# Performance work log

Measured on AMD Instinct MI355X. Metric: run time of the kernel, lower is better.

## Reference

```python
import jax, jax.numpy as jnp
import numpy as np

N = 50000      # nodes (cells)
E = 800000     # directed edges
IN, H1, H2, Z = 512, 128, 128, 64


def setup_inputs() -> dict:
    key = jax.random.key(0)
    ks = jax.random.split(key, 12)
    x = jax.random.normal(ks[0], (N, IN), jnp.float32)
    edge_index = jax.random.randint(ks[1], (2, E), 0, N, dtype=jnp.int64)

    def glorot(k, i, o):
        return jax.random.normal(k, (i, o), jnp.float32) * np.float32(1.0 / np.sqrt(i))

    return {
        "x": x,
        "edge_index": edge_index,
        "W1": glorot(ks[2], IN, H1), "b1": jnp.zeros((H1,), jnp.float32),
        "W2": glorot(ks[3], H1, H2), "b2": jnp.zeros((H2,), jnp.float32),
        "Wm": glorot(ks[4], H2, Z),  "bm": jnp.zeros((Z,), jnp.float32),
        "Ws": glorot(ks[5], H2, Z),  "bs": jnp.zeros((Z,), jnp.float32),
    }


def _gcn_norm(edge_index, n):
    # PyG GCNConv default: add self-loops, sym-normalize D^-1/2 (A+I) D^-1/2
    loops = jnp.arange(n, dtype=edge_index.dtype)
    src = jnp.concatenate([edge_index[0], loops])
    dst = jnp.concatenate([edge_index[1], loops])
    deg = jax.ops.segment_sum(jnp.ones_like(dst, jnp.float32), dst, num_segments=n)
    dis = jnp.where(deg > 0, jax.lax.rsqrt(jnp.maximum(deg, 1.0)), 0.0)
    norm = dis[src] * dis[dst]  # [E+N]
    return src, dst, norm


def _gcn_conv(x, W, b, src, dst, norm, n):
    h = x @ W                          # [N, out] transform first
    msg = h[src] * norm[:, None]       # gather + scale
    out = jax.ops.segment_sum(msg, dst, num_segments=n)  # scatter-add at targets
    return out + b


def reference(x, edge_index, W1, b1, W2, b2, Wm, bm, Ws, bs):
    n = x.shape[0]
    src, dst, norm = _gcn_norm(edge_index, n)
    h = jax.nn.relu(_gcn_conv(x, W1, b1, src, dst, norm, n))
    h = jax.nn.relu(_gcn_conv(h, W2, b2, src, dst, norm, n))
    # dropout p=0.4 is identity in eval mode
    z_mean = _gcn_conv(h, Wm, bm, src, dst, norm, n)
    z_log_std = _gcn_conv(h, Ws, bs, src, dst, norm, n)
    return (z_mean, z_log_std)
```

## Files before the change

kernel.cpp:

```cpp
#include <hip/hip_runtime.h>


using u16 = unsigned short;
typedef __attribute__((ext_vector_type(8))) short short8;
typedef __attribute__((ext_vector_type(4))) float f32x4;

__device__ __forceinline__ void split_bf16(float f, u16& hi, u16& lo) {
    unsigned b = __float_as_uint(f);
    hi = (u16)(b >> 16);
    float rem = f - __uint_as_float(b & 0xFFFF0000u);
    lo = (u16)(__float_as_uint(rem) >> 16);
}

__device__ __forceinline__ int block_mode(const int* __restrict__ ew, int* sflag) {
    if (threadIdx.x == 0) *sflag = 0;
    __syncthreads();
    if (ew[2 * (int)threadIdx.x + 1] != 0) atomicOr(sflag, 1);
    __syncthreads();
    return *sflag ? 0 : 1;
}

__global__ void deg_kernel(const int* __restrict__ ew, int* __restrict__ deg, int E) {
    __shared__ int sflag;
    int mode = block_mode(ew, &sflag);
    int e = blockIdx.x * blockDim.x + threadIdx.x;
    if (e >= E) return;
    int d = mode ? ew[2 * E + 2 * e] : ew[E + e];
    atomicAdd(&deg[d], 1);
}

__global__ void scan_block_kernel(const int* __restrict__ deg, int* __restrict__ rowptr,
                                  int* __restrict__ aux, float* __restrict__ dis, int N) {
    __shared__ int s[256];
    int i = blockIdx.x * 256 + threadIdx.x;
    int v = (i < N) ? deg[i] : 0;
    if (i < N) dis[i] = rsqrtf((float)v + 1.0f);
    s[threadIdx.x] = v;
    __syncthreads();
    for (int off = 1; off < 256; off <<= 1) {
        int t = (threadIdx.x >= off) ? s[threadIdx.x - off] : 0;
        __syncthreads();
        s[threadIdx.x] += t;
        __syncthreads();
    }
    if (i < N) rowptr[i] = s[threadIdx.x] - v;
    if (threadIdx.x == 255) aux[blockIdx.x] = s[255];
}

__global__ void scan_aux_kernel(int* __restrict__ aux, int nb) {
    __shared__ int s[256];
    int i = threadIdx.x;
    int v = (i < nb) ? aux[i] : 0;
    s[i] = v;
    __syncthreads();
    for (int off = 1; off < 256; off <<= 1) {
        int t = (i >= off) ? s[i - off] : 0;
        __syncthreads();
        s[i] += t;
        __syncthreads();
    }
    if (i < nb) aux[i] = s[i] - v;
}

__global__ void add_offsets_kernel(int* __restrict__ rowptr, const int* __restrict__ aux,
                                   int N, int E) {
    int i = blockIdx.x * 256 + threadIdx.x;
    if (i < N) rowptr[i] += aux[i >> 8];
    if (i == 0) rowptr[N] = E;
}

__global__ void fill_csr_kernel(const int* __restrict__ ew,
                                const int* __restrict__ rowptr, int* __restrict__ cursor,
                                int* __restrict__ csr_src, int E) {
    __shared__ int sflag;
    int mode = block_mode(ew, &sflag);
    int e = blockIdx.x * blockDim.x + threadIdx.x;
    if (e >= E) return;
    int s = mode ? ew[2 * e] : ew[e];
    int d = mode ? ew[2 * E + 2 * e] : ew[E + e];
    int pos = rowptr[d] + atomicAdd(&cursor[d], 1);
    csr_src[pos] = s;
}

__global__ void conv_all_kernel(const float* __restrict__ W1, const float* __restrict__ W2,
                                const float* __restrict__ Wm, const float* __restrict__ Ws,
                                u16* __restrict__ W1t_hi, u16* __restrict__ W1t_lo,
                                u16* __restrict__ W2t_hi, u16* __restrict__ W2t_lo,
                                u16* __restrict__ Wct_hi, u16* __restrict__ Wct_lo) {
    int idx = blockIdx.x * 256 + threadIdx.x;
    u16 h, l;
    if (idx < 65536) {
        int k = idx >> 7, n = idx & 127;
        split_bf16(W1[idx], h, l);
        W1t_hi[n * 512 + k] = h;
        W1t_lo[n * 512 + k] = l;
    } else if (idx < 81920) {
        int t = idx - 65536;
        int k = t >> 7, n = t & 127;
        split_bf16(W2[t], h, l);
        W2t_hi[n * 128 + k] = h;
        W2t_lo[n * 128 + k] = l;
    } else if (idx < 98304) {
        int t = idx - 81920;
        int k = t >> 7, j = t & 127;
        float f = (j < 64) ? Wm[k * 64 + j] : Ws[k * 64 + (j - 64)];
        split_bf16(f, h, l);
        Wct_hi[j * 128 + k] = h;
        Wct_lo[j * 128 + k] = l;
    }
}

#define TILE_OFF(t) ((t) * 520)

__global__ __launch_bounds__(256) void gemm_mfma(const float* __restrict__ A,
                                                 const u16* __restrict__ Bt_hi,
                                                 const u16* __restrict__ Bt_lo,
                                                 float* __restrict__ C,
                                                 int N, int K) {
    __shared__ u16 AsH[4 * 520], AsL[4 * 520];
    __shared__ u16 BsH[8 * 520], BsL[8 * 520];

    const int tid = threadIdx.x;
    const int w = tid >> 6, lane = tid & 63;
    const int row0 = blockIdx.y * 64;

    const int s_ar = w * 16 + (lane & 15);
    const int s_ak = (lane >> 4) * 8;
    const int a_dst = TILE_OFF(w) + lane * 8;
    const int s_bc = tid >> 1;
    const int s_bk = (tid & 1) * 16;
    const int b_q0 = (tid & 1) * 2;
    const int b_dst0 = TILE_OFF(s_bc >> 4) + ((s_bc & 15) + 16 * (b_q0 + 0)) * 8;
    const int b_dst1 = TILE_OFF(s_bc >> 4) + ((s_bc & 15) + 16 * (b_q0 + 1)) * 8;

    const int R = (w >> 1) * 32, Cc = (w & 1) * 64;
    const int atile = (w >> 1) * 2;
    const int btile = (w & 1) * 4;
    const int m16 = lane & 15, quad = lane >> 4;

    f32x4 acc[2][4];
#pragma unroll
    for (int i = 0; i < 2; ++i)
#pragma unroll
        for (int j = 0; j < 4; ++j) acc[i][j] = (f32x4)0.f;

    const int grow = row0 + s_ar;
    const bool ok = (grow < N);
    const float* aptr = A + (size_t)grow * K + s_ak;
    const u16* bph = Bt_hi + (size_t)s_bc * K + s_bk;
    const u16* bpl = Bt_lo + (size_t)s_bc * K + s_bk;

    float av[8];
    short8 rbh0, rbh1, rbl0, rbl1;
    {
        f32x4 v0 = (f32x4)0.f, v1 = (f32x4)0.f;
        if (ok) { v0 = *(const f32x4*)&aptr[0]; v1 = *(const f32x4*)&aptr[4]; }
#pragma unroll
        for (int q = 0; q < 4; ++q) { av[q] = v0[q]; av[4 + q] = v1[q]; }
        rbh0 = *(const short8*)&bph[0];
        rbh1 = *(const short8*)&bph[8];
        rbl0 = *(const short8*)&bpl[0];
        rbl1 = *(const short8*)&bpl[8];
    }

    const int ksteps = K >> 5;
    for (int ks = 0; ks < ksteps; ++ks) {
        short8 ah, al;
#pragma unroll
        for (int q = 0; q < 8; ++q) {
            u16 h, l;
            split_bf16(av[q], h, l);
            ah[q] = (short)h;
            al[q] = (short)l;
        }
        __syncthreads();
        *(short8*)&AsH[a_dst] = ah;
        *(short8*)&AsL[a_dst] = al;
        *(short8*)&BsH[b_dst0] = rbh0;
        *(short8*)&BsH[b_dst1] = rbh1;
        *(short8*)&BsL[b_dst0] = rbl0;
        *(short8*)&BsL[b_dst1] = rbl1;
        __syncthreads();

        if (ks + 1 < ksteps) {
            const int k0 = (ks + 1) * 32;
            f32x4 v0 = (f32x4)0.f, v1 = (f32x4)0.f;
            if (ok) { v0 = *(const f32x4*)&aptr[k0]; v1 = *(const f32x4*)&aptr[k0 + 4]; }
#pragma unroll
            for (int q = 0; q < 4; ++q) { av[q] = v0[q]; av[4 + q] = v1[q]; }
            rbh0 = *(const short8*)&bph[k0];
            rbh1 = *(const short8*)&bph[k0 + 8];
            rbl0 = *(const short8*)&bpl[k0];
            rbl1 = *(const short8*)&bpl[k0 + 8];
        }

        short8 fa_h[2], fa_l[2], fb_h[4], fb_l[4];
#pragma unroll
        for (int i = 0; i < 2; ++i) {
            fa_h[i] = *(const short8*)&AsH[TILE_OFF(atile + i) + lane * 8];
            fa_l[i] = *(const short8*)&AsL[TILE_OFF(atile + i) + lane * 8];
        }
#pragma unroll
        for (int j = 0; j < 4; ++j) {
            fb_h[j] = *(const short8*)&BsH[TILE_OFF(btile + j) + lane * 8];
            fb_l[j] = *(const short8*)&BsL[TILE_OFF(btile + j) + lane * 8];
        }
#pragma unroll
        for (int i = 0; i < 2; ++i)
#pragma unroll
            for (int j = 0; j < 4; ++j) {
                acc[i][j] = __builtin_amdgcn_mfma_f32_16x16x32_bf16(
                    fa_h[i], fb_h[j], acc[i][j], 0, 0, 0);
                acc[i][j] = __builtin_amdgcn_mfma_f32_16x16x32_bf16(
                    fa_h[i], fb_l[j], acc[i][j], 0, 0, 0);
                acc[i][j] = __builtin_amdgcn_mfma_f32_16x16x32_bf16(
                    fa_l[i], fb_h[j], acc[i][j], 0, 0, 0);
            }
    }

#pragma unroll
    for (int i = 0; i < 2; ++i) {
#pragma unroll
        for (int r = 0; r < 4; ++r) {
            int gr = row0 + R + i * 16 + quad * 4 + r;
            if (gr < N) {
#pragma unroll
                for (int j = 0; j < 4; ++j)
                    C[(size_t)gr * 128 + Cc + j * 16 + m16] = acc[i][j][r];
            }
        }
    }
}

__global__ __launch_bounds__(256) void propagate_kernel(
    const float* __restrict__ h, const int* __restrict__ rowptr,
    const int* __restrict__ csr_src, const float* __restrict__ dis,
    const float* __restrict__ bias, float* __restrict__ out, int N, int do_relu) {
    int wave = (blockIdx.x * 256 + threadIdx.x) >> 6;
    int lane = threadIdx.x & 63;
    if (wave >= N) return;
    int v = wave;
    int f = lane * 2;
    float dv = dis[v];
    float ax = 0.f, ay = 0.f;
    int beg = rowptr[v], end = rowptr[v + 1];
    int i = beg;
    for (; i + 8 <= end; i += 8) {
        int s[8];
        float ww[8];
        float2 g[8];
#pragma unroll
        for (int u = 0; u < 8; ++u) s[u] = csr_src[i + u];
#pragma unroll
        for (int u = 0; u < 8; ++u) ww[u] = dis[s[u]];
#pragma unroll
        for (int u = 0; u < 8; ++u) g[u] = *(const float2*)&h[(size_t)s[u] * 128 + f];
#pragma unroll
        for (int u = 0; u < 8; ++u) {
            float t = ww[u] * dv;
            ax += t * g[u].x;
            ay += t * g[u].y;
        }
    }
    if (i + 4 <= end) {
        int s[4];
        float ww[4];
        float2 g[4];
#pragma unroll
        for (int u = 0; u < 4; ++u) s[u] = csr_src[i + u];
#pragma unroll
        for (int u = 0; u < 4; ++u) ww[u] = dis[s[u]];
#pragma unroll
        for (int u = 0; u < 4; ++u) g[u] = *(const float2*)&h[(size_t)s[u] * 128 + f];
#pragma unroll
        for (int u = 0; u < 4; ++u) {
            float t = ww[u] * dv;
            ax += t * g[u].x;
            ay += t * g[u].y;
        }
        i += 4;
    }
    for (; i < end; ++i) {
        int s = csr_src[i];
        float ws = dis[s] * dv;
        float2 g = *(const float2*)&h[(size_t)s * 128 + f];
        ax += ws * g.x;
        ay += ws * g.y;
    }
    float2 hv = *(const float2*)&h[(size_t)v * 128 + f];
    ax += dv * dv * hv.x;
    ay += dv * dv * hv.y;
    ax += bias[f];
    ay += bias[f + 1];
    if (do_relu) { ax = fmaxf(ax, 0.f); ay = fmaxf(ay, 0.f); }
    *(float2*)&out[(size_t)v * 128 + f] = make_float2(ax, ay);
}

__global__ __launch_bounds__(256) void propagate_final_kernel(
    const float* __restrict__ h, const int* __restrict__ rowptr,
    const int* __restrict__ csr_src, const float* __restrict__ dis,
    const float* __restrict__ bm, const float* __restrict__ bs,
    float* __restrict__ out, int N) {
    int wave = (blockIdx.x * 256 + threadIdx.x) >> 6;
    int lane = threadIdx.x & 63;
    if (wave >= N) return;
    int v = wave;
    int f = lane * 2;
    float dv = dis[v];
    float ax = 0.f, ay = 0.f;
    int beg = rowptr[v], end = rowptr[v + 1];
    int i = beg;
    for (; i + 8 <= end; i += 8) {
        int s[8];
        float ww[8];
        float2 g[8];
#pragma unroll
        for (int u = 0; u < 8; ++u) s[u] = csr_src[i + u];
#pragma unroll
        for (int u = 0; u < 8; ++u) ww[u] = dis[s[u]];
#pragma unroll
        for (int u = 0; u < 8; ++u) g[u] = *(const float2*)&h[(size_t)s[u] * 128 + f];
#pragma unroll
        for (int u = 0; u < 8; ++u) {
            float t = ww[u] * dv;
            ax += t * g[u].x;
            ay += t * g[u].y;
        }
    }
    if (i + 4 <= end) {
        int s[4];
        float ww[4];
        float2 g[4];
#pragma unroll
        for (int u = 0; u < 4; ++u) s[u] = csr_src[i + u];
#pragma unroll
        for (int u = 0; u < 4; ++u) ww[u] = dis[s[u]];
#pragma unroll
        for (int u = 0; u < 4; ++u) g[u] = *(const float2*)&h[(size_t)s[u] * 128 + f];
#pragma unroll
        for (int u = 0; u < 4; ++u) {
            float t = ww[u] * dv;
            ax += t * g[u].x;
            ay += t * g[u].y;
        }
        i += 4;
    }
    for (; i < end; ++i) {
        int s = csr_src[i];
        float ws = dis[s] * dv;
        float2 g = *(const float2*)&h[(size_t)s * 128 + f];
        ax += ws * g.x;
        ay += ws * g.y;
    }
    float2 hv = *(const float2*)&h[(size_t)v * 128 + f];
    ax += dv * dv * hv.x;
    ay += dv * dv * hv.y;
    if (f < 64) {
        *(float2*)&out[(size_t)v * 64 + f] = make_float2(ax + bm[f], ay + bm[f + 1]);
    } else {
        int g = f - 64;
        *(float2*)&out[(size_t)N * 64 + (size_t)v * 64 + g] =
            make_float2(ax + bs[g], ay + bs[g + 1]);
    }
}

extern "C" void kernel_launch(void* const* d_in, const int* in_sizes, int n_in,
                              void* d_out, int out_size, void* d_ws, size_t ws_size,
                              hipStream_t stream) {
    const float* x  = (const float*)d_in[0];
    const int*   ew = (const int*)d_in[1];
    const float* W1 = (const float*)d_in[2];
    const float* b1 = (const float*)d_in[3];
    const float* W2 = (const float*)d_in[4];
    const float* b2 = (const float*)d_in[5];
    const float* Wm = (const float*)d_in[6];
    const float* bm = (const float*)d_in[7];
    const float* Ws = (const float*)d_in[8];
    const float* bs = (const float*)d_in[9];
    float* out = (float*)d_out;

    const int IN = 512, H = 128;
    const int N = in_sizes[0] / IN;
    const int E = in_sizes[1] / 2;

    char* base = (char*)d_ws;
    size_t off = 0;
    auto alloc = [&](size_t bytes) -> char* {
        char* p = base + off;
        off = (off + bytes + 255) & ~(size_t)255;
        return p;
    };
    char*  degcur  = (char*) alloc(400384);
    float* dis     = (float*)alloc((size_t)N * 4);
    int*   rowptr  = (int*)  alloc((size_t)(N + 1) * 4);
    int*   aux     = (int*)  alloc(256 * 4);
    int*   csr_src = (int*)  alloc((size_t)E * 4);
    u16*   W1t_hi  = (u16*)  alloc((size_t)IN * H * 2);
    u16*   W1t_lo  = (u16*)  alloc((size_t)IN * H * 2);
    u16*   W2t_hi  = (u16*)  alloc((size_t)H * H * 2);
    u16*   W2t_lo  = (u16*)  alloc((size_t)H * H * 2);
    u16*   Wct_hi  = (u16*)  alloc((size_t)H * H * 2);
    u16*   Wct_lo  = (u16*)  alloc((size_t)H * H * 2);
    float* hA      = (float*)alloc((size_t)N * H * 4);
    float* hB      = (float*)alloc((size_t)N * H * 4);
    (void)ws_size; (void)n_in; (void)out_size;

    int* deg    = (int*)degcur;
    int* cursor = (int*)(degcur + 200192);

    hipMemsetAsync(degcur, 0, 400384, stream);

    const int eblocks = (E + 255) / 256;
    const int nblocks = (N + 255) / 256;

    conv_all_kernel<<<(98304 + 255) / 256, 256, 0, stream>>>(
        W1, W2, Wm, Ws, W1t_hi, W1t_lo, W2t_hi, W2t_lo, Wct_hi, Wct_lo);
    deg_kernel<<<eblocks, 256, 0, stream>>>(ew, deg, E);
    scan_block_kernel<<<nblocks, 256, 0, stream>>>(deg, rowptr, aux, dis, N);
    scan_aux_kernel<<<1, 256, 0, stream>>>(aux, nblocks);
    add_offsets_kernel<<<nblocks, 256, 0, stream>>>(rowptr, aux, N, E);
    fill_csr_kernel<<<eblocks, 256, 0, stream>>>(ew, rowptr, cursor, csr_src, E);

    dim3 gg(1, (N + 63) / 64);
    const int pblocks = (N * 64 + 255) / 256;

    gemm_mfma<<<gg, 256, 0, stream>>>(x, W1t_hi, W1t_lo, hA, N, IN);
    propagate_kernel<<<pblocks, 256, 0, stream>>>(hA, rowptr, csr_src, dis,
                                                  b1, hB, N, 1);
    gemm_mfma<<<gg, 256, 0, stream>>>(hB, W2t_hi, W2t_lo, hA, N, H);
    propagate_kernel<<<pblocks, 256, 0, stream>>>(hA, rowptr, csr_src, dis,
                                                  b2, hB, N, 1);
    gemm_mfma<<<gg, 256, 0, stream>>>(hB, Wct_hi, Wct_lo, hA, N, H);
    propagate_final_kernel<<<pblocks, 256, 0, stream>>>(hA, rowptr, csr_src, dis,
                                                        bm, bs, out, N);
}
```

Baseline: 494.3 us.

## Drop LDS staging in GEMM; load MFMA fragments directly per wave

The GEMM no longer stages A and B through shared memory with block-wide barriers. Each wave now owns its own 32x64 output tile, loads its A rows and pre-split B columns straight from global memory into MFMA fragment registers, and double-buffers the A loads across k-steps. This removes the __syncthreads and LDS traffic. In exchange, data reuse between waves is lost: B fragments are reloaded by every wave and A rows are read by two waves, which shifts more load onto the L2/L1 caches. The loop assumes an even number of k-steps, which holds for K of 512 and 128.

```diff
diff --git a/kernel.cpp b/kernel.cpp
--- a/kernel.cpp
+++ b/kernel.cpp
@@ -110,123 +110,104 @@
     }
 }
 
-#define TILE_OFF(t) ((t) * 520)
-
 __global__ __launch_bounds__(256) void gemm_mfma(const float* __restrict__ A,
                                                  const u16* __restrict__ Bt_hi,
                                                  const u16* __restrict__ Bt_lo,
                                                  float* __restrict__ C,
                                                  int N, int K) {
-    __shared__ u16 AsH[4 * 520], AsL[4 * 520];
-    __shared__ u16 BsH[8 * 520], BsL[8 * 520];
-
     const int tid = threadIdx.x;
     const int w = tid >> 6, lane = tid & 63;
-    const int row0 = blockIdx.y * 64;
-
-    const int s_ar = w * 16 + (lane & 15);
-    const int s_ak = (lane >> 4) * 8;
-    const int a_dst = TILE_OFF(w) + lane * 8;
-    const int s_bc = tid >> 1;
-    const int s_bk = (tid & 1) * 16;
-    const int b_q0 = (tid & 1) * 2;
-    const int b_dst0 = TILE_OFF(s_bc >> 4) + ((s_bc & 15) + 16 * (b_q0 + 0)) * 8;
-    const int b_dst1 = TILE_OFF(s_bc >> 4) + ((s_bc & 15) + 16 * (b_q0 + 1)) * 8;
-
-    const int R = (w >> 1) * 32, Cc = (w & 1) * 64;
-    const int atile = (w >> 1) * 2;
-    const int btile = (w & 1) * 4;
     const int m16 = lane & 15, quad = lane >> 4;
 
+    const int nrt = (N + 31) >> 5;
+    const int wtile = blockIdx.x * 4 + w;
+    if (wtile >= 2 * nrt) return;
+    const int rt = wtile >> 1;
+    const int c0 = (wtile & 1) << 6;
+    const int row0 = rt << 5;
+
+    int r0 = row0 + m16;      if (r0 > N - 1) r0 = N - 1;
+    int r1 = row0 + 16 + m16; if (r1 > N - 1) r1 = N - 1;
+    const float* ap0 = A + (size_t)r0 * K + quad * 8;
+    const float* ap1 = A + (size_t)r1 * K + quad * 8;
+    const u16* bph = Bt_hi + (size_t)(c0 + m16) * K + quad * 8;
+    const u16* bpl = Bt_lo + (size_t)(c0 + m16) * K + quad * 8;
+    const size_t bstr = (size_t)16 * K;
+
     f32x4 acc[2][4];
 #pragma unroll
     for (int i = 0; i < 2; ++i)
 #pragma unroll
         for (int j = 0; j < 4; ++j) acc[i][j] = (f32x4)0.f;
 
-    const int grow = row0 + s_ar;
-    const bool ok = (grow < N);
-    const float* aptr = A + (size_t)grow * K + s_ak;
-    const u16* bph = Bt_hi + (size_t)s_bc * K + s_bk;
-    const u16* bpl = Bt_lo + (size_t)s_bc * K + s_bk;
-
-    float av[8];
-    short8 rbh0, rbh1, rbl0, rbl1;
-    {
-        f32x4 v0 = (f32x4)0.f, v1 = (f32x4)0.f;
-        if (ok) { v0 = *(const f32x4*)&aptr[0]; v1 = *(const f32x4*)&aptr[4]; }
-#pragma unroll
-        for (int q = 0; q < 4; ++q) { av[q] = v0[q]; av[4 + q] = v1[q]; }
-        rbh0 = *(const short8*)&bph[0];
-        rbh1 = *(const short8*)&bph[8];
-        rbl0 = *(const short8*)&bpl[0];
-        rbl1 = *(const short8*)&bpl[8];
-    }
-
-    const int ksteps = K >> 5;
-    for (int ks = 0; ks < ksteps; ++ks) {
-        short8 ah, al;
-#pragma unroll
-        for (int q = 0; q < 8; ++q) {
-            u16 h, l;
-            split_bf16(av[q], h, l);
-            ah[q] = (short)h;
-            al[q] = (short)l;
-        }
-        __syncthreads();
-        *(short8*)&AsH[a_dst] = ah;
-        *(short8*)&AsL[a_dst] = al;
-        *(short8*)&BsH[b_dst0] = rbh0;
-        *(short8*)&BsH[b_dst1] = rbh1;
-        *(short8*)&BsL[b_dst0] = rbl0;
-        *(short8*)&BsL[b_dst1] = rbl1;
-        __syncthreads();
-
-        if (ks + 1 < ksteps) {
-            const int k0 = (ks + 1) * 32;
-            f32x4 v0 = (f32x4)0.f, v1 = (f32x4)0.f;
-            if (ok) { v0 = *(const f32x4*)&aptr[k0]; v1 = *(const f32x4*)&aptr[k0 + 4]; }
-#pragma unroll
-            for (int q = 0; q < 4; ++q) { av[q] = v0[q]; av[4 + q] = v1[q]; }
-            rbh0 = *(const short8*)&bph[k0];
-            rbh1 = *(const short8*)&bph[k0 + 8];
-            rbl0 = *(const short8*)&bpl[k0];
-            rbl1 = *(const short8*)&bpl[k0 + 8];
-        }
-
-        short8 fa_h[2], fa_l[2], fb_h[4], fb_l[4];
-#pragma unroll
-        for (int i = 0; i < 2; ++i) {
-            fa_h[i] = *(const short8*)&AsH[TILE_OFF(atile + i) + lane * 8];
-            fa_l[i] = *(const short8*)&AsL[TILE_OFF(atile + i) + lane * 8];
-        }
+    f32x4 x0, x1, x2, x3;
+    f32x4 y0, y1, y2, y3;
+
+    auto lda = [&](f32x4& v0, f32x4& v1, f32x4& v2, f32x4& v3, int kk) {
+        const float* p0 = ap0 + kk * 32;
+        const float* p1 = ap1 + kk * 32;
+        v0 = *(const f32x4*)p0;
+        v1 = *(const f32x4*)(p0 + 4);
+        v2 = *(const f32x4*)p1;
+        v3 = *(const f32x4*)(p1 + 4);
+    };
+    auto cvt = [&](const f32x4& v0, const f32x4& v1, short8& h, short8& l) {
+#pragma unroll
+        for (int q = 0; q < 4; ++q) {
+            u16 hh, ll;
+            split_bf16(v0[q], hh, ll);
+            h[q] = (short)hh;
+            l[q] = (short)ll;
+            split_bf16(v1[q], hh, ll);
+            h[4 + q] = (short)hh;
+            l[4 + q] = (short)ll;
+        }
+    };
+    auto step = [&](f32x4& v0, f32x4& v1, f32x4& v2, f32x4& v3,
+                    int kk, int kpre, bool pre) {
+        short8 bh[4], bl[4];
 #pragma unroll
         for (int j = 0; j < 4; ++j) {
-            fb_h[j] = *(const short8*)&BsH[TILE_OFF(btile + j) + lane * 8];
-            fb_l[j] = *(const short8*)&BsL[TILE_OFF(btile + j) + lane * 8];
-        }
+            bh[j] = *(const short8*)(bph + bstr * j + kk * 32);
+            bl[j] = *(const short8*)(bpl + bstr * j + kk * 32);
+        }
+        short8 ah[2], al[2];
+        cvt(v0, v1, ah[0], al[0]);
+        cvt(v2, v3, ah[1], al[1]);
+        if (pre) lda(v0, v1, v2, v3, kpre);
 #pragma unroll
         for (int i = 0; i < 2; ++i)
 #pragma unroll
             for (int j = 0; j < 4; ++j) {
                 acc[i][j] = __builtin_amdgcn_mfma_f32_16x16x32_bf16(
-                    fa_h[i], fb_h[j], acc[i][j], 0, 0, 0);
+                    ah[i], bh[j], acc[i][j], 0, 0, 0);
                 acc[i][j] = __builtin_amdgcn_mfma_f32_16x16x32_bf16(
-                    fa_h[i], fb_l[j], acc[i][j], 0, 0, 0);
+                    ah[i], bl[j], acc[i][j], 0, 0, 0);
                 acc[i][j] = __builtin_amdgcn_mfma_f32_16x16x32_bf16(
-                    fa_l[i], fb_h[j], acc[i][j], 0, 0, 0);
+                    al[i], bh[j], acc[i][j], 0, 0, 0);
             }
-    }
+    };
+
+    const int ksteps = K >> 5;
+    lda(x0, x1, x2, x3, 0);
+    lda(y0, y1, y2, y3, 1);
+    int ks = 0;
+    for (; ks + 2 < ksteps; ks += 2) {
+        step(x0, x1, x2, x3, ks, ks + 2, true);
+        step(y0, y1, y2, y3, ks + 1, ks + 3, true);
+    }
+    step(x0, x1, x2, x3, ks, 0, false);
+    step(y0, y1, y2, y3, ks + 1, 0, false);
 
 #pragma unroll
     for (int i = 0; i < 2; ++i) {
 #pragma unroll
         for (int r = 0; r < 4; ++r) {
-            int gr = row0 + R + i * 16 + quad * 4 + r;
+            int gr = row0 + i * 16 + quad * 4 + r;
             if (gr < N) {
 #pragma unroll
                 for (int j = 0; j < 4; ++j)
-                    C[(size_t)gr * 128 + Cc + j * 16 + m16] = acc[i][j][r];
+                    C[(size_t)gr * 128 + c0 + j * 16 + m16] = acc[i][j][r];
             }
         }
     }
@@ -421,16 +402,17 @@
     add_offsets_kernel<<<nblocks, 256, 0, stream>>>(rowptr, aux, N, E);
     fill_csr_kernel<<<eblocks, 256, 0, stream>>>(ew, rowptr, cursor, csr_src, E);
 
-    dim3 gg(1, (N + 63) / 64);
+    const int wtiles = 2 * ((N + 31) / 32);
+    const int gblocks = (wtiles + 3) / 4;
     const int pblocks = (N * 64 + 255) / 256;
 
-    gemm_mfma<<<gg, 256, 0, stream>>>(x, W1t_hi, W1t_lo, hA, N, IN);
+    gemm_mfma<<<gblocks, 256, 0, stream>>>(x, W1t_hi, W1t_lo, hA, N, IN);
     propagate_kernel<<<pblocks, 256, 0, stream>>>(hA, rowptr, csr_src, dis,
                                                   b1, hB, N, 1);
-    gemm_mfma<<<gg, 256, 0, stream>>>(hB, W2t_hi, W2t_lo, hA, N, H);
+    gemm_mfma<<<gblocks, 256, 0, stream>>>(hB, W2t_hi, W2t_lo, hA, N, H);
     propagate_kernel<<<pblocks, 256, 0, stream>>>(hA, rowptr, csr_src, dis,
                                                   b2, hB, N, 1);
-    gemm_mfma<<<gg, 256, 0, stream>>>(hB, Wct_hi, Wct_lo, hA, N, H);
+    gemm_mfma<<<gblocks, 256, 0, stream>>>(hB, Wct_hi, Wct_lo, hA, N, H);
     propagate_final_kernel<<<pblocks, 256, 0, stream>>>(hA, rowptr, csr_src, dis,
                                                         bm, bs, out, N);
 }
```

Result: slower. 551.3 us (+11.5%).

## Shrink GEMM row tile to 32 rows with 1D grid and per-wave column split

Applied to the files above, without the earlier changes.

The MFMA GEMM now processes 32 rows per block instead of 64, and each of the four waves computes a 32x32 output slice covering all 32 rows. A-tile loading uses one float4 per thread with the row index clamped instead of predicated. The block count doubles to fill more CUs with fewer accumulators per wave. In exchange the B tile (the full 128-column weight slice) is reloaded by twice as many blocks, raising weight traffic per output row.

```diff
diff --git a/kernel.cpp b/kernel.cpp
--- a/kernel.cpp
+++ b/kernel.cpp
@@ -3,6 +3,7 @@
 
 using u16 = unsigned short;
 typedef __attribute__((ext_vector_type(8))) short short8;
+typedef __attribute__((ext_vector_type(4))) short short4v;
 typedef __attribute__((ext_vector_type(4))) float f32x4;
 
 __device__ __forceinline__ void split_bf16(float f, u16& hi, u16& lo) {
@@ -117,65 +118,60 @@
                                                  const u16* __restrict__ Bt_lo,
                                                  float* __restrict__ C,
                                                  int N, int K) {
-    __shared__ u16 AsH[4 * 520], AsL[4 * 520];
-    __shared__ u16 BsH[8 * 520], BsL[8 * 520];
+    __shared__ __align__(16) u16 AsH[2 * 520], AsL[2 * 520];
+    __shared__ __align__(16) u16 BsH[8 * 520], BsL[8 * 520];
 
     const int tid = threadIdx.x;
     const int w = tid >> 6, lane = tid & 63;
-    const int row0 = blockIdx.y * 64;
-
-    const int s_ar = w * 16 + (lane & 15);
-    const int s_ak = (lane >> 4) * 8;
-    const int a_dst = TILE_OFF(w) + lane * 8;
+    const int m16 = lane & 15, quad = lane >> 4;
+    const int row0 = blockIdx.x * 32;
+
+    const int s_ar = tid & 31;
+    const int s_ac = tid >> 5;
+    int ar = row0 + s_ar; if (ar > N - 1) ar = N - 1;
+    const float* aptr = A + (size_t)ar * K + s_ac * 4;
+    const int a_dst = TILE_OFF(s_ar >> 4) + ((s_ac >> 1) * 16 + (s_ar & 15)) * 8
+                      + (s_ac & 1) * 4;
+
     const int s_bc = tid >> 1;
     const int s_bk = (tid & 1) * 16;
     const int b_q0 = (tid & 1) * 2;
     const int b_dst0 = TILE_OFF(s_bc >> 4) + ((s_bc & 15) + 16 * (b_q0 + 0)) * 8;
     const int b_dst1 = TILE_OFF(s_bc >> 4) + ((s_bc & 15) + 16 * (b_q0 + 1)) * 8;
-
-    const int R = (w >> 1) * 32, Cc = (w & 1) * 64;
-    const int atile = (w >> 1) * 2;
-    const int btile = (w & 1) * 4;
-    const int m16 = lane & 15, quad = lane >> 4;
-
-    f32x4 acc[2][4];
-#pragma unroll
-    for (int i = 0; i < 2; ++i)
-#pragma unroll
-        for (int j = 0; j < 4; ++j) acc[i][j] = (f32x4)0.f;
-
-    const int grow = row0 + s_ar;
-    const bool ok = (grow < N);
-    const float* aptr = A + (size_t)grow * K + s_ak;
     const u16* bph = Bt_hi + (size_t)s_bc * K + s_bk;
     const u16* bpl = Bt_lo + (size_t)s_bc * K + s_bk;
 
-    float av[8];
+    const int btile = w * 2;
+
+    f32x4 acc[2][2];
+#pragma unroll
+    for (int i = 0; i < 2; ++i)
+#pragma unroll
+        for (int j = 0; j < 2; ++j) acc[i][j] = (f32x4)0.f;
+
+    f32x4 av;
     short8 rbh0, rbh1, rbl0, rbl1;
-    {
-        f32x4 v0 = (f32x4)0.f, v1 = (f32x4)0.f;
-        if (ok) { v0 = *(const f32x4*)&aptr[0]; v1 = *(const f32x4*)&aptr[4]; }
-#pragma unroll
-        for (int q = 0; q < 4; ++q) { av[q] = v0[q]; av[4 + q] = v1[q]; }
-        rbh0 = *(const short8*)&bph[0];
-        rbh1 = *(const short8*)&bph[8];
-        rbl0 = *(const short8*)&bpl[0];
-        rbl1 = *(const short8*)&bpl[8];
-    }
 
     const int ksteps = K >> 5;
+
+    av = *(const f32x4*)&aptr[0];
+    rbh0 = *(const short8*)&bph[0];
+    rbh1 = *(const short8*)&bph[8];
+    rbl0 = *(const short8*)&bpl[0];
+    rbl1 = *(const short8*)&bpl[8];
+
     for (int ks = 0; ks < ksteps; ++ks) {
-        short8 ah, al;
-#pragma unroll
-        for (int q = 0; q < 8; ++q) {
-            u16 h, l;
-            split_bf16(av[q], h, l);
-            ah[q] = (short)h;
-            al[q] = (short)l;
-        }
-        __syncthreads();
-        *(short8*)&AsH[a_dst] = ah;
-        *(short8*)&AsL[a_dst] = al;
+        short4v ah4, al4;
+#pragma unroll
+        for (int q = 0; q < 4; ++q) {
+            u16 hh, ll;
+            split_bf16(av[q], hh, ll);
+            ah4[q] = (short)hh;
+            al4[q] = (short)ll;
+        }
+        __syncthreads();
+        *(short4v*)&AsH[a_dst] = ah4;
+        *(short4v*)&AsL[a_dst] = al4;
         *(short8*)&BsH[b_dst0] = rbh0;
         *(short8*)&BsH[b_dst1] = rbh1;
         *(short8*)&BsL[b_dst0] = rbl0;
@@ -184,37 +180,35 @@
 
         if (ks + 1 < ksteps) {
             const int k0 = (ks + 1) * 32;
-            f32x4 v0 = (f32x4)0.f, v1 = (f32x4)0.f;
-            if (ok) { v0 = *(const f32x4*)&aptr[k0]; v1 = *(const f32x4*)&aptr[k0 + 4]; }
-#pragma unroll
-            for (int q = 0; q < 4; ++q) { av[q] = v0[q]; av[4 + q] = v1[q]; }
+            av = *(const f32x4*)&aptr[k0];
             rbh0 = *(const short8*)&bph[k0];
             rbh1 = *(const short8*)&bph[k0 + 8];
             rbl0 = *(const short8*)&bpl[k0];
             rbl1 = *(const short8*)&bpl[k0 + 8];
         }
 
-        short8 fa_h[2], fa_l[2], fb_h[4], fb_l[4];
+        short8 fah[2], fal[2], fbh[2], fbl[2];
 #pragma unroll
         for (int i = 0; i < 2; ++i) {
-            fa_h[i] = *(const short8*)&AsH[TILE_OFF(atile + i) + lane * 8];
-            fa_l[i] = *(const short8*)&AsL[TILE_OFF(atile + i) + lane * 8];
-        }
-#pragma unroll
-        for (int j = 0; j < 4; ++j) {
-            fb_h[j] = *(const short8*)&BsH[TILE_OFF(btile + j) + lane * 8];
-            fb_l[j] = *(const short8*)&BsL[TILE_OFF(btile + j) + lane * 8];
-        }
+            fah[i] = *(const short8*)&AsH[TILE_OFF(i) + lane * 8];
+            fal[i] = *(const short8*)&AsL[TILE_OFF(i) + lane * 8];
+        }
+#pragma unroll
+        for (int j = 0; j < 2; ++j) {
+            fbh[j] = *(const short8*)&BsH[TILE_OFF(btile + j) + lane * 8];
+            fbl[j] = *(const short8*)&BsL[TILE_OFF(btile + j) + lane * 8];
+        }
+
 #pragma unroll
         for (int i = 0; i < 2; ++i)
 #pragma unroll
-            for (int j = 0; j < 4; ++j) {
+            for (int j = 0; j < 2; ++j) {
                 acc[i][j] = __builtin_amdgcn_mfma_f32_16x16x32_bf16(
-                    fa_h[i], fb_h[j], acc[i][j], 0, 0, 0);
+                    fah[i], fbh[j], acc[i][j], 0, 0, 0);
                 acc[i][j] = __builtin_amdgcn_mfma_f32_16x16x32_bf16(
-                    fa_h[i], fb_l[j], acc[i][j], 0, 0, 0);
+                    fah[i], fbl[j], acc[i][j], 0, 0, 0);
                 acc[i][j] = __builtin_amdgcn_mfma_f32_16x16x32_bf16(
-                    fa_l[i], fb_h[j], acc[i][j], 0, 0, 0);
+                    fal[i], fbh[j], acc[i][j], 0, 0, 0);
             }
     }
 
@@ -222,11 +216,11 @@
     for (int i = 0; i < 2; ++i) {
 #pragma unroll
         for (int r = 0; r < 4; ++r) {
-            int gr = row0 + R + i * 16 + quad * 4 + r;
+            int gr = row0 + i * 16 + quad * 4 + r;
             if (gr < N) {
 #pragma unroll
-                for (int j = 0; j < 4; ++j)
-                    C[(size_t)gr * 128 + Cc + j * 16 + m16] = acc[i][j][r];
+                for (int j = 0; j < 2; ++j)
+                    C[(size_t)gr * 128 + w * 32 + j * 16 + m16] = acc[i][j][r];
             }
         }
     }
@@ -296,7 +290,7 @@
     *(float2*)&out[(size_t)v * 128 + f] = make_float2(ax, ay);
 }
 
-__global__ __launch_bounds__(256) void propagate_final_kernel(
+__global__ void __launch_bounds__(256) propagate_final_kernel(
     const float* __restrict__ h, const int* __restrict__ rowptr,
     const int* __restrict__ csr_src, const float* __restrict__ dis,
     const float* __restrict__ bm, const float* __restrict__ bs,
@@ -421,16 +415,16 @@
     add_offsets_kernel<<<nblocks, 256, 0, stream>>>(rowptr, aux, N, E);
     fill_csr_kernel<<<eblocks, 256, 0, stream>>>(ew, rowptr, cursor, csr_src, E);
 
-    dim3 gg(1, (N + 63) / 64);
+    const int gblocks = (N + 31) / 32;
     const int pblocks = (N * 64 + 255) / 256;
 
-    gemm_mfma<<<gg, 256, 0, stream>>>(x, W1t_hi, W1t_lo, hA, N, IN);
+    gemm_mfma<<<gblocks, 256, 0, stream>>>(x, W1t_hi, W1t_lo, hA, N, IN);
     propagate_kernel<<<pblocks, 256, 0, stream>>>(hA, rowptr, csr_src, dis,
                                                   b1, hB, N, 1);
-    gemm_mfma<<<gg, 256, 0, stream>>>(hB, W2t_hi, W2t_lo, hA, N, H);
+    gemm_mfma<<<gblocks, 256, 0, stream>>>(hB, W2t_hi, W2t_lo, hA, N, H);
     propagate_kernel<<<pblocks, 256, 0, stream>>>(hA, rowptr, csr_src, dis,
                                                   b2, hB, N, 1);
-    gemm_mfma<<<gg, 256, 0, stream>>>(hB, Wct_hi, Wct_lo, hA, N, H);
+    gemm_mfma<<<gblocks, 256, 0, stream>>>(hB, Wct_hi, Wct_lo, hA, N, H);
     propagate_final_kernel<<<pblocks, 256, 0, stream>>>(hA, rowptr, csr_src, dis,
                                                         bm, bs, out, N);
 }
```

After: 524.3 us. +6.1%, slower.

## Pre-swizzle weights into MFMA fragment layout and load B directly from global

Applied to the files above, without the earlier changes.

The weight conversion kernel now writes the split bf16 hi/lo weights in the exact per-lane MFMA fragment order. The GEMM then loads its B fragments straight from global/L2 into registers and no longer stages B through shared memory. This removes the B LDS writes and reads and shrinks shared memory per block, which may raise occupancy. In exchange, each wave issues uncached-prefetch global loads for B every k-step inside the loop, with no software prefetch, so it relies on L2 hits.

```diff
diff --git a/kernel.cpp b/kernel.cpp
--- a/kernel.cpp
+++ b/kernel.cpp
@@ -84,59 +84,72 @@
 
 __global__ void conv_all_kernel(const float* __restrict__ W1, const float* __restrict__ W2,
                                 const float* __restrict__ Wm, const float* __restrict__ Ws,
-                                u16* __restrict__ W1t_hi, u16* __restrict__ W1t_lo,
-                                u16* __restrict__ W2t_hi, u16* __restrict__ W2t_lo,
-                                u16* __restrict__ Wct_hi, u16* __restrict__ Wct_lo) {
+                                u16* __restrict__ B1h, u16* __restrict__ B1l,
+                                u16* __restrict__ B2h, u16* __restrict__ B2l,
+                                u16* __restrict__ Bch, u16* __restrict__ Bcl) {
     int idx = blockIdx.x * 256 + threadIdx.x;
     u16 h, l;
     if (idx < 65536) {
-        int k = idx >> 7, n = idx & 127;
-        split_bf16(W1[idx], h, l);
-        W1t_hi[n * 512 + k] = h;
-        W1t_lo[n * 512 + k] = l;
+        int t = idx >> 13;
+        int ks = (idx >> 9) & 15;
+        int L = (idx >> 3) & 63;
+        int q = idx & 7;
+        int col = t * 16 + (L & 15);
+        int k = ks * 32 + (L >> 4) * 8 + q;
+        split_bf16(W1[k * 128 + col], h, l);
+        B1h[idx] = h;
+        B1l[idx] = l;
     } else if (idx < 81920) {
-        int t = idx - 65536;
-        int k = t >> 7, n = t & 127;
-        split_bf16(W2[t], h, l);
-        W2t_hi[n * 128 + k] = h;
-        W2t_lo[n * 128 + k] = l;
+        int o = idx - 65536;
+        int t = o >> 11;
+        int ks = (o >> 9) & 3;
+        int L = (o >> 3) & 63;
+        int q = o & 7;
+        int col = t * 16 + (L & 15);
+        int k = ks * 32 + (L >> 4) * 8 + q;
+        split_bf16(W2[k * 128 + col], h, l);
+        B2h[o] = h;
+        B2l[o] = l;
     } else if (idx < 98304) {
-        int t = idx - 81920;
-        int k = t >> 7, j = t & 127;
-        float f = (j < 64) ? Wm[k * 64 + j] : Ws[k * 64 + (j - 64)];
+        int o = idx - 81920;
+        int t = o >> 11;
+        int ks = (o >> 9) & 3;
+        int L = (o >> 3) & 63;
+        int q = o & 7;
+        int col = t * 16 + (L & 15);
+        int k = ks * 32 + (L >> 4) * 8 + q;
+        float f = (col < 64) ? Wm[k * 64 + col] : Ws[k * 64 + (col - 64)];
         split_bf16(f, h, l);
-        Wct_hi[j * 128 + k] = h;
-        Wct_lo[j * 128 + k] = l;
+        Bch[o] = h;
+        Bcl[o] = l;
     }
 }
 
 #define TILE_OFF(t) ((t) * 520)
 
 __global__ __launch_bounds__(256) void gemm_mfma(const float* __restrict__ A,
-                                                 const u16* __restrict__ Bt_hi,
-                                                 const u16* __restrict__ Bt_lo,
+                                                 const u16* __restrict__ Bfh,
+                                                 const u16* __restrict__ Bfl,
                                                  float* __restrict__ C,
                                                  int N, int K) {
-    __shared__ u16 AsH[4 * 520], AsL[4 * 520];
-    __shared__ u16 BsH[8 * 520], BsL[8 * 520];
+    __shared__ __align__(16) u16 AsH[4 * 520], AsL[4 * 520];
 
     const int tid = threadIdx.x;
     const int w = tid >> 6, lane = tid & 63;
-    const int row0 = blockIdx.y * 64;
+    const int m16 = lane & 15, quad = lane >> 4;
+    const int row0 = blockIdx.x * 64;
 
     const int s_ar = w * 16 + (lane & 15);
     const int s_ak = (lane >> 4) * 8;
     const int a_dst = TILE_OFF(w) + lane * 8;
-    const int s_bc = tid >> 1;
-    const int s_bk = (tid & 1) * 16;
-    const int b_q0 = (tid & 1) * 2;
-    const int b_dst0 = TILE_OFF(s_bc >> 4) + ((s_bc & 15) + 16 * (b_q0 + 0)) * 8;
-    const int b_dst1 = TILE_OFF(s_bc >> 4) + ((s_bc & 15) + 16 * (b_q0 + 1)) * 8;
 
     const int R = (w >> 1) * 32, Cc = (w & 1) * 64;
     const int atile = (w >> 1) * 2;
     const int btile = (w & 1) * 4;
-    const int m16 = lane & 15, quad = lane >> 4;
+
+    const int ksteps = K >> 5;
+    const u16* bfh = Bfh + ((size_t)btile * ksteps) * 512 + lane * 8;
+    const u16* bfl = Bfl + ((size_t)btile * ksteps) * 512 + lane * 8;
 
     f32x4 acc[2][4];
 #pragma unroll
@@ -147,24 +160,23 @@
     const int grow = row0 + s_ar;
     const bool ok = (grow < N);
     const float* aptr = A + (size_t)grow * K + s_ak;
-    const u16* bph = Bt_hi + (size_t)s_bc * K + s_bk;
-    const u16* bpl = Bt_lo + (size_t)s_bc * K + s_bk;
 
     float av[8];
-    short8 rbh0, rbh1, rbl0, rbl1;
     {
         f32x4 v0 = (f32x4)0.f, v1 = (f32x4)0.f;
         if (ok) { v0 = *(const f32x4*)&aptr[0]; v1 = *(const f32x4*)&aptr[4]; }
 #pragma unroll
         for (int q = 0; q < 4; ++q) { av[q] = v0[q]; av[4 + q] = v1[q]; }
-        rbh0 = *(const short8*)&bph[0];
-        rbh1 = *(const short8*)&bph[8];
-        rbl0 = *(const short8*)&bpl[0];
-        rbl1 = *(const short8*)&bpl[8];
-    }
-
-    const int ksteps = K >> 5;
+    }
+
     for (int ks = 0; ks < ksteps; ++ks) {
+        short8 fbh[4], fbl[4];
+#pragma unroll
+        for (int j = 0; j < 4; ++j) {
+            fbh[j] = *(const short8*)(bfh + (size_t)(j * ksteps + ks) * 512);
+            fbl[j] = *(const short8*)(bfl + (size_t)(j * ksteps + ks) * 512);
+        }
+
         short8 ah, al;
 #pragma unroll
         for (int q = 0; q < 8; ++q) {
@@ -176,10 +188,6 @@
         __syncthreads();
         *(short8*)&AsH[a_dst] = ah;
         *(short8*)&AsL[a_dst] = al;
-        *(short8*)&BsH[b_dst0] = rbh0;
-        *(short8*)&BsH[b_dst1] = rbh1;
-        *(short8*)&BsL[b_dst0] = rbl0;
-        *(short8*)&BsL[b_dst1] = rbl1;
         __syncthreads();
 
         if (ks + 1 < ksteps) {
@@ -188,33 +196,25 @@
             if (ok) { v0 = *(const f32x4*)&aptr[k0]; v1 = *(const f32x4*)&aptr[k0 + 4]; }
 #pragma unroll
             for (int q = 0; q < 4; ++q) { av[q] = v0[q]; av[4 + q] = v1[q]; }
-            rbh0 = *(const short8*)&bph[k0];
-            rbh1 = *(const short8*)&bph[k0 + 8];
-            rbl0 = *(const short8*)&bpl[k0];
-            rbl1 = *(const short8*)&bpl[k0 + 8];
-        }
-
-        short8 fa_h[2], fa_l[2], fb_h[4], fb_l[4];
+        }
+
+        short8 fah[2], fal[2];
 #pragma unroll
         for (int i = 0; i < 2; ++i) {
-            fa_h[i] = *(const short8*)&AsH[TILE_OFF(atile + i) + lane * 8];
-            fa_l[i] = *(const short8*)&AsL[TILE_OFF(atile + i) + lane * 8];
-        }
-#pragma unroll
-        for (int j = 0; j < 4; ++j) {
-            fb_h[j] = *(const short8*)&BsH[TILE_OFF(btile + j) + lane * 8];
-            fb_l[j] = *(const short8*)&BsL[TILE_OFF(btile + j) + lane * 8];
-        }
+            fah[i] = *(const short8*)&AsH[TILE_OFF(atile + i) + lane * 8];
+            fal[i] = *(const short8*)&AsL[TILE_OFF(atile + i) + lane * 8];
+        }
+
 #pragma unroll
         for (int i = 0; i < 2; ++i)
 #pragma unroll
             for (int j = 0; j < 4; ++j) {
                 acc[i][j] = __builtin_amdgcn_mfma_f32_16x16x32_bf16(
-                    fa_h[i], fb_h[j], acc[i][j], 0, 0, 0);
+                    fah[i], fbh[j], acc[i][j], 0, 0, 0);
                 acc[i][j] = __builtin_amdgcn_mfma_f32_16x16x32_bf16(
-                    fa_h[i], fb_l[j], acc[i][j], 0, 0, 0);
+                    fah[i], fbl[j], acc[i][j], 0, 0, 0);
                 acc[i][j] = __builtin_amdgcn_mfma_f32_16x16x32_bf16(
-                    fa_l[i], fb_h[j], acc[i][j], 0, 0, 0);
+                    fal[i], fbh[j], acc[i][j], 0, 0, 0);
             }
     }
 
@@ -296,7 +296,7 @@
     *(float2*)&out[(size_t)v * 128 + f] = make_float2(ax, ay);
 }
 
-__global__ __launch_bounds__(256) void propagate_final_kernel(
+__global__ void __launch_bounds__(256) propagate_final_kernel(
     const float* __restrict__ h, const int* __restrict__ rowptr,
     const int* __restrict__ csr_src, const float* __restrict__ dis,
     const float* __restrict__ bm, const float* __restrict__ bs,
@@ -395,12 +395,12 @@
     int*   rowptr  = (int*)  alloc((size_t)(N + 1) * 4);
     int*   aux     = (int*)  alloc(256 * 4);
     int*   csr_src = (int*)  alloc((size_t)E * 4);
-    u16*   W1t_hi  = (u16*)  alloc((size_t)IN * H * 2);
-    u16*   W1t_lo  = (u16*)  alloc((size_t)IN * H * 2);
-    u16*   W2t_hi  = (u16*)  alloc((size_t)H * H * 2);
-    u16*   W2t_lo  = (u16*)  alloc((size_t)H * H * 2);
-    u16*   Wct_hi  = (u16*)  alloc((size_t)H * H * 2);
-    u16*   Wct_lo  = (u16*)  alloc((size_t)H * H * 2);
+    u16*   B1h     = (u16*)  alloc((size_t)IN * H * 2);
+    u16*   B1l     = (u16*)  alloc((size_t)IN * H * 2);
+    u16*   B2h     = (u16*)  alloc((size_t)H * H * 2);
+    u16*   B2l     = (u16*)  alloc((size_t)H * H * 2);
+    u16*   Bch     = (u16*)  alloc((size_t)H * H * 2);
+    u16*   Bcl     = (u16*)  alloc((size_t)H * H * 2);
     float* hA      = (float*)alloc((size_t)N * H * 4);
     float* hB      = (float*)alloc((size_t)N * H * 4);
     (void)ws_size; (void)n_in; (void)out_size;
@@ -414,23 +414,23 @@
     const int nblocks = (N + 255) / 256;
 
     conv_all_kernel<<<(98304 + 255) / 256, 256, 0, stream>>>(
-        W1, W2, Wm, Ws, W1t_hi, W1t_lo, W2t_hi, W2t_lo, Wct_hi, Wct_lo);
+        W1, W2, Wm, Ws, B1h, B1l, B2h, B2l, Bch, Bcl);
     deg_kernel<<<eblocks, 256, 0, stream>>>(ew, deg, E);
     scan_block_kernel<<<nblocks, 256, 0, stream>>>(deg, rowptr, aux, dis, N);
     scan_aux_kernel<<<1, 256, 0, stream>>>(aux, nblocks);
     add_offsets_kernel<<<nblocks, 256, 0, stream>>>(rowptr, aux, N, E);
     fill_csr_kernel<<<eblocks, 256, 0, stream>>>(ew, rowptr, cursor, csr_src, E);
 
-    dim3 gg(1, (N + 63) / 64);
+    const int gblocks = (N + 63) / 64;
     const int pblocks = (N * 64 + 255) / 256;
 
-    gemm_mfma<<<gg, 256, 0, stream>>>(x, W1t_hi, W1t_lo, hA, N, IN);
+    gemm_mfma<<<gblocks, 256, 0, stream>>>(x, B1h, B1l, hA, N, IN);
     propagate_kernel<<<pblocks, 256, 0, stream>>>(hA, rowptr, csr_src, dis,
                                                   b1, hB, N, 1);
-    gemm_mfma<<<gg, 256, 0, stream>>>(hB, W2t_hi, W2t_lo, hA, N, H);
+    gemm_mfma<<<gblocks, 256, 0, stream>>>(hB, B2h, B2l, hA, N, H);
     propagate_kernel<<<pblocks, 256, 0, stream>>>(hA, rowptr, csr_src, dis,
                                                   b2, hB, N, 1);
-    gemm_mfma<<<gg, 256, 0, stream>>>(hB, Wct_hi, Wct_lo, hA, N, H);
+    gemm_mfma<<<gblocks, 256, 0, stream>>>(hB, Bch, Bcl, hA, N, H);
     propagate_final_kernel<<<pblocks, 256, 0, stream>>>(hA, rowptr, csr_src, dis,
                                                         bm, bs, out, N);
 }
```

Result: no change. 484.7 us (-1.9%).
